# Performance work log

Hardware: AMD Instinct MI355X
Metric: run time of the kernel (lower is better)

The kernel has to match this reference:

```python
import jax, jax.numpy as jnp
import numpy as np

N, H, K, T, B, IN_DIM, L = 1024, 64, 2, 12, 8, 2, 2
NNZ = 16384  # N * avg_degree(16)
M = 2 * K + 1  # supports_len * max_diffusion_step + 1 = 5


def setup_inputs() -> dict:
    key = jax.random.key(0)
    ks = jax.random.split(key, 13)

    def xavier(k, shape):
        std = 1.414 * (2.0 / (shape[0] + shape[1])) ** 0.5
        return std * jax.random.normal(k, shape, dtype=jnp.float32)

    F0 = IN_DIM + H  # 66
    F1 = 2 * H       # 128
    return {
        "inputs": jax.random.normal(ks[0], (T, B, N * IN_DIM), dtype=jnp.float32),
        "initial_hidden_state": jnp.zeros((L, B, N * H), dtype=jnp.float32),
        "support_rows": jax.random.randint(ks[1], (2, NNZ), 0, N, dtype=jnp.int32),
        "support_cols": jax.random.randint(ks[2], (2, NNZ), 0, N, dtype=jnp.int32),
        # scale like a random-walk-normalized adjacency (avg degree ~16)
        "support_vals": jax.random.uniform(ks[3], (2, NNZ), dtype=jnp.float32) / 16.0,
        "Wg0": xavier(ks[4], (F0 * M, 2 * H)),
        "bg0": 0.01 * jax.random.normal(ks[5], (2 * H,), dtype=jnp.float32),
        "Wc0": xavier(ks[6], (F0 * M, H)),
        "bc0": 0.01 * jax.random.normal(ks[7], (H,), dtype=jnp.float32),
        "Wg1": xavier(ks[8], (F1 * M, 2 * H)),
        "bg1": 0.01 * jax.random.normal(ks[9], (2 * H,), dtype=jnp.float32),
        "Wc1": xavier(ks[10], (F1 * M, H)),
        "bc1": 0.01 * jax.random.normal(ks[11], (H,), dtype=jnp.float32),
    }


def reference(inputs, initial_hidden_state, support_rows, support_cols, support_vals,
              Wg0, bg0, Wc0, bc0, Wg1, bg1, Wc1, bc1):
    supports = [(support_rows[i], support_cols[i], support_vals[i])
                for i in range(support_rows.shape[0])]

    def spmm(rows, cols, vals, x):  # sparse [N,N] @ x[N,FB]
        return jax.ops.segment_sum(vals[:, None] * x[cols], rows, num_segments=N)

    def diffuse(x):  # x: [B, N, F] -> [B*N, F*M] (Chebyshev-style recurrence)
        Bz, _, F = x.shape
        x0 = x.transpose(1, 2, 0).reshape(N, F * Bz)
        mats = [x0]
        for rows, cols, vals in supports:
            x1 = spmm(rows, cols, vals, x0)
            mats.append(x1)
            xkm2, xkm1 = x0, x1
            for _ in range(2, K + 1):
                xk = 2.0 * spmm(rows, cols, vals, xkm1) - xkm2
                mats.append(xk)
                xkm2, xkm1 = xkm1, xk
        Xs = jnp.stack(mats, 0).reshape(len(mats), N, F, Bz)
        return Xs.transpose(3, 1, 2, 0).reshape(Bz * N, F * len(mats))

    def cell(params, inp_t, state):  # one DCGRU step
        Wg, bg, Wc, bc = params
        Bz = inp_t.shape[0]
        xi = inp_t.reshape(Bz, N, -1)
        gates = jax.nn.sigmoid(
            diffuse(jnp.concatenate([xi, state.reshape(Bz, N, H)], 2)) @ Wg + bg
        ).reshape(Bz, N, 2 * H)
        r = gates[..., :H].reshape(Bz, N * H)
        u = gates[..., H:].reshape(Bz, N * H)
        cand_in = jnp.concatenate([xi, (r * state).reshape(Bz, N, H)], 2)
        c = jnp.tanh((diffuse(cand_in) @ Wc + bc).reshape(Bz, N * H))
        return u * state + (1.0 - u) * c

    layer_params = [(Wg0, bg0, Wc0, bc0), (Wg1, bg1, Wc1, bc1)]
    cur = inputs  # [T, B, N*input_dim]
    hiddens = []
    for l, params in enumerate(layer_params):
        def step(state, x_t, params=params):
            ns = cell(params, x_t, state)
            return ns, ns
        h_last, outs = jax.lax.scan(step, initial_hidden_state[l], cur)
        hiddens.append(h_last)
        cur = outs  # [T, B, N*H]
    return jnp.stack(hiddens, 0), cur
```

## Files before the change

kernel.cpp:

```cpp
#include <hip/hip_runtime.h>
#include <hip/hip_bf16.h>
#include <math.h>

#define NN 1024
#define HH 64
#define TT 12
#define BB 8
#define INDIM 2
#define LL 2
#define NNZE 16384
#define MM 5

#define FP0 96
#define FP1 128
#define CP0 (BB * FP0)
#define CP1 (BB * FP1)

static constexpr size_t BNH = (size_t)BB * NN * HH;

typedef short bf16x8 __attribute__((ext_vector_type(8)));
typedef float f32x4 __attribute__((ext_vector_type(4)));

__device__ __forceinline__ void fma4(float4& acc, float v, const float4& p) {
  acc.x += v * p.x;
  acc.y += v * p.y;
  acc.z += v * p.z;
  acc.w += v * p.w;
}
__device__ __forceinline__ void mul4(float4& a, const float4& g) {
  a.x *= g.x; a.y *= g.y; a.z *= g.z; a.w *= g.w;
}

__global__ void zero_int_kernel(int* p, int n) {
  int i = blockIdx.x * blockDim.x + threadIdx.x;
  if (i < n) p[i] = 0;
}

__global__ void copy_kernel(const float* __restrict__ src, float* __restrict__ dst, int n) {
  int i = blockIdx.x * blockDim.x + threadIdx.x;
  if (i < n) dst[i] = src[i];
}

__global__ void csr_count_kernel(const int* __restrict__ rows, int* __restrict__ counts) {
  int i = blockIdx.x * blockDim.x + threadIdx.x;
  if (i < 2 * NNZE) {
    int s = i / NNZE;
    atomicAdd(&counts[s * NN + rows[i]], 1);
  }
}

__global__ void csr_scan_kernel(const int* __restrict__ counts, int* __restrict__ row_start,
                                int* __restrict__ cursor) {
  __shared__ int bufA[NN];
  __shared__ int bufB[NN];
  int s = blockIdx.x;
  int t = threadIdx.x;
  bufA[t] = counts[s * NN + t];
  __syncthreads();
  int* src = bufA;
  int* dst = bufB;
  for (int off = 1; off < NN; off <<= 1) {
    dst[t] = src[t] + (t >= off ? src[t - off] : 0);
    __syncthreads();
    int* tmp = src; src = dst; dst = tmp;
  }
  row_start[s * (NN + 1) + t + 1] = src[t];
  cursor[s * NN + t] = (t == 0) ? 0 : src[t - 1];
  if (t == 0) row_start[s * (NN + 1)] = 0;
}

__global__ void csr_scatter_kernel(const int* __restrict__ rows, const int* __restrict__ colsIn,
                                   const float* __restrict__ valsIn, int* __restrict__ cursor,
                                   int* __restrict__ colsOut, float* __restrict__ valsOut) {
  int i = blockIdx.x * blockDim.x + threadIdx.x;
  if (i < 2 * NNZE) {
    int s = i / NNZE;
    int r = rows[i];
    int pos = atomicAdd(&cursor[s * NN + r], 1);
    colsOut[s * NNZE + pos] = colsIn[i];
    valsOut[s * NNZE + pos] = valsIn[i];
  }
}

__global__ void permwT_kernel(const float* __restrict__ W, unsigned short* __restrict__ WTh,
                              unsigned short* __restrict__ WTl, int F, int Fp, int J, int reord) {
  int Ktot = MM * Fp;
  int total = J * Ktot;
  for (int idx = blockIdx.x * blockDim.x + threadIdx.x; idx < total;
       idx += gridDim.x * blockDim.x) {
    int k = idx % Ktot;
    int j = idx / Ktot;
    int m = k / Fp;
    int fn = k - m * Fp;
    int fo;
    if (reord) {
      fo = (fn < HH) ? fn + INDIM : (fn < HH + INDIM ? fn - HH : -1);
    } else {
      fo = (fn < F) ? fn : -1;
    }
    float x = (fo >= 0) ? W[(size_t)(fo * MM + m) * J + j] : 0.f;
    unsigned u = __float_as_uint(x);
    WTh[idx] = (unsigned short)(u >> 16);
    float hf = __uint_as_float(u & 0xFFFF0000u);
    WTl[idx] = (unsigned short)(__float_as_uint(x - hf) >> 16);
  }
}

__global__ __launch_bounds__(256) void spmm1_l1_kernel(
    const int* __restrict__ row_start, const int* __restrict__ cols,
    const float* __restrict__ vals, const float* __restrict__ xi,
    const float* __restrict__ state,
    float* __restrict__ mats) {
  const int r = blockIdx.x, s = blockIdx.y, tid = threadIdx.x;
  const int b = tid >> 5;
  const int f = (tid & 31) * 4;
  const bool isX = (f < HH);
  const float* src = isX ? xi : state;
  const float* sb = src + (size_t)b * NN * HH + (isX ? f : f - HH);

  const int* rs = row_start + s * (NN + 1);
  const int* cs = cols + s * NNZE;
  const float* vs = vals + s * NNZE;
  const int start = rs[r], end = rs[r + 1];

  float4 a0 = {0, 0, 0, 0}, a1 = {0, 0, 0, 0}, a2 = {0, 0, 0, 0}, a3 = {0, 0, 0, 0};
  int e = start;
  for (; e + 3 < end; e += 4) {
    int c0 = cs[e], c1 = cs[e + 1], c2 = cs[e + 2], c3 = cs[e + 3];
    float v0 = vs[e], v1 = vs[e + 1], v2 = vs[e + 2], v3 = vs[e + 3];
    float4 x0 = *(const float4*)(sb + (size_t)c0 * HH);
    float4 x1 = *(const float4*)(sb + (size_t)c1 * HH);
    float4 x2 = *(const float4*)(sb + (size_t)c2 * HH);
    float4 x3 = *(const float4*)(sb + (size_t)c3 * HH);
    fma4(a0, v0, x0); fma4(a1, v1, x1); fma4(a2, v2, x2); fma4(a3, v3, x3);
  }
  for (; e < end; ++e) {
    int c0 = cs[e];
    float v0 = vs[e];
    float4 x0 = *(const float4*)(sb + (size_t)c0 * HH);
    fma4(a0, v0, x0);
  }
  float4 o;
  o.x = (a0.x + a1.x) + (a2.x + a3.x);
  o.y = (a0.y + a1.y) + (a2.y + a3.y);
  o.z = (a0.z + a1.z) + (a2.z + a3.z);
  o.w = (a0.w + a1.w) + (a2.w + a3.w);
  *(float4*)(mats + (size_t)(1 + 2 * s) * (NN * CP1) + (size_t)r * CP1 + tid * 4) = o;

  if (s == 0) {
    *(float4*)(mats + (size_t)r * CP1 + tid * 4) = *(const float4*)(sb + (size_t)r * HH);
  }
}

__global__ __launch_bounds__(256) void spmm1_l0_kernel(
    const int* __restrict__ row_start, const int* __restrict__ cols,
    const float* __restrict__ vals, const float* __restrict__ xi,
    const float* __restrict__ state,
    float* __restrict__ mats) {
  const int tid = threadIdx.x;
  constexpr int SLOTS = FP0 / 4;
  if (tid >= BB * SLOTS) return;
  const int r = blockIdx.x, s = blockIdx.y;
  const int b = tid / SLOTS;
  const int fn = (tid - b * SLOTS) * 4;
  const int c4 = b * FP0 + fn;

  float* x1p = mats + (size_t)(1 + 2 * s) * (NN * CP0) + (size_t)r * CP0 + c4;
  float* x0p = mats + (size_t)r * CP0 + c4;

  const int* rs = row_start + s * (NN + 1);
  const int* cs = cols + s * NNZE;
  const float* vs = vals + s * NNZE;
  const int start = rs[r], end = rs[r + 1];

  if (fn < HH) {
    const float* sb = state + (size_t)b * NN * HH + fn;
    float4 a0 = {0, 0, 0, 0}, a1 = {0, 0, 0, 0}, a2 = {0, 0, 0, 0}, a3 = {0, 0, 0, 0};
    int e = start;
    for (; e + 3 < end; e += 4) {
      int c0 = cs[e], c1 = cs[e + 1], c2 = cs[e + 2], c3 = cs[e + 3];
      float v0 = vs[e], v1 = vs[e + 1], v2 = vs[e + 2], v3 = vs[e + 3];
      float4 x0 = *(const float4*)(sb + (size_t)c0 * HH);
      float4 x1 = *(const float4*)(sb + (size_t)c1 * HH);
      float4 x2 = *(const float4*)(sb + (size_t)c2 * HH);
      float4 x3 = *(const float4*)(sb + (size_t)c3 * HH);
      fma4(a0, v0, x0); fma4(a1, v1, x1); fma4(a2, v2, x2); fma4(a3, v3, x3);
    }
    for (; e < end; ++e) {
      int c0 = cs[e];
      float v0 = vs[e];
      float4 x0 = *(const float4*)(sb + (size_t)c0 * HH);
      fma4(a0, v0, x0);
    }
    float4 o;
    o.x = (a0.x + a1.x) + (a2.x + a3.x);
    o.y = (a0.y + a1.y) + (a2.y + a3.y);
    o.z = (a0.z + a1.z) + (a2.z + a3.z);
    o.w = (a0.w + a1.w) + (a2.w + a3.w);
    *(float4*)x1p = o;
    if (s == 0) *(float4*)x0p = *(const float4*)(sb + (size_t)r * HH);
  } else if (fn == HH) {
    const float* xb = xi + (size_t)b * NN * INDIM;
    float p0 = 0.f, p1 = 0.f, q0 = 0.f, q1 = 0.f;
    int e = start;
    for (; e + 1 < end; e += 2) {
      int c0 = cs[e], c1 = cs[e + 1];
      float v0 = vs[e], v1 = vs[e + 1];
      p0 += v0 * xb[(size_t)c0 * INDIM];
      q0 += v0 * xb[(size_t)c0 * INDIM + 1];
      p1 += v1 * xb[(size_t)c1 * INDIM];
      q1 += v1 * xb[(size_t)c1 * INDIM + 1];
    }
    if (e < end) {
      int c0 = cs[e];
      float v0 = vs[e];
      p0 += v0 * xb[(size_t)c0 * INDIM];
      q0 += v0 * xb[(size_t)c0 * INDIM + 1];
    }
    float4 o = {p0 + p1, q0 + q1, 0.f, 0.f};
    *(float4*)x1p = o;
    if (s == 0) {
      float4 x = {xb[(size_t)r * INDIM], xb[(size_t)r * INDIM + 1], 0.f, 0.f};
      *(float4*)x0p = x;
    }
  } else {
    float4 z = {0, 0, 0, 0};
    *(float4*)x1p = z;
    if (s == 0) *(float4*)x0p = z;
  }
}

template <int LAYER>
__global__ __launch_bounds__(256) void spmm1_state_kernel(
    const int* __restrict__ row_start, const int* __restrict__ cols,
    const float* __restrict__ vals, const float* __restrict__ state,
    const float* __restrict__ gates, float* __restrict__ mats) {
  constexpr int FPP = (LAYER == 0) ? FP0 : FP1;
  constexpr int CP = BB * FPP;
  constexpr int BASE = (LAYER == 0) ? 0 : HH;
  const int tid = threadIdx.x;
  const int r = blockIdx.x * 2 + (tid >> 7);
  const int slot = tid & 127;
  const int b = slot >> 4;
  const int fi = (slot & 15) * 4;
  const int s = blockIdx.y;

  const float* sb = state + (size_t)b * NN * HH + fi;
  const float* gb = gates + (size_t)b * NN * (2 * HH) + fi;

  const int* rs = row_start + s * (NN + 1);
  const int* cs = cols + s * NNZE;
  const float* vs = vals + s * NNZE;
  const int start = rs[r], end = rs[r + 1];

  float4 a0 = {0, 0, 0, 0}, a1 = {0, 0, 0, 0}, a2 = {0, 0, 0, 0}, a3 = {0, 0, 0, 0};
  int e = start;
  for (; e + 3 < end; e += 4) {
    int c0 = cs[e], c1 = cs[e + 1], c2 = cs[e + 2], c3 = cs[e + 3];
    float v0 = vs[e], v1 = vs[e + 1], v2 = vs[e + 2], v3 = vs[e + 3];
    float4 x0 = *(const float4*)(sb + (size_t)c0 * HH);
    float4 g0 = *(const float4*)(gb + (size_t)c0 * (2 * HH));
    float4 x1 = *(const float4*)(sb + (size_t)c1 * HH);
    float4 g1 = *(const float4*)(gb + (size_t)c1 * (2 * HH));
    float4 x2 = *(const float4*)(sb + (size_t)c2 * HH);
    float4 g2 = *(const float4*)(gb + (size_t)c2 * (2 * HH));
    float4 x3 = *(const float4*)(sb + (size_t)c3 * HH);
    float4 g3 = *(const float4*)(gb + (size_t)c3 * (2 * HH));
    mul4(x0, g0); mul4(x1, g1); mul4(x2, g2); mul4(x3, g3);
    fma4(a0, v0, x0); fma4(a1, v1, x1); fma4(a2, v2, x2); fma4(a3, v3, x3);
  }
  for (; e < end; ++e) {
    int c0 = cs[e];
    float v0 = vs[e];
    float4 x0 = *(const float4*)(sb + (size_t)c0 * HH);
    float4 g0 = *(const float4*)(gb + (size_t)c0 * (2 * HH));
    mul4(x0, g0);
    fma4(a0, v0, x0);
  }
  float4 o;
  o.x = (a0.x + a1.x) + (a2.x + a3.x);
  o.y = (a0.y + a1.y) + (a2.y + a3.y);
  o.z = (a0.z + a1.z) + (a2.z + a3.z);
  o.w = (a0.w + a1.w) + (a2.w + a3.w);
  const int c4 = b * FPP + BASE + fi;
  *(float4*)(mats + (size_t)(1 + 2 * s) * (NN * CP) + (size_t)r * CP + c4) = o;

  if (s == 0) {
    float4 x = *(const float4*)(sb + (size_t)r * HH);
    float4 g = *(const float4*)(gb + (size_t)r * (2 * HH));
    mul4(x, g);
    *(float4*)(mats + (size_t)r * CP + c4) = x;
  }
}

template <int LAYER>
__global__ __launch_bounds__(256) void spmm2_kernel(
    const int* __restrict__ row_start, const int* __restrict__ cols,
    const float* __restrict__ vals, float* __restrict__ mats) {
  constexpr int FPP = (LAYER == 0) ? FP0 : FP1;
  constexpr int CPX = BB * FPP;
  const int tid = threadIdx.x;
  int c4, fn;
  if (LAYER == 0) {
    constexpr int SLOTS = FP0 / 4;
    if (tid >= BB * SLOTS) return;
    const int b = tid / SLOTS;
    fn = (tid - b * SLOTS) * 4;
    c4 = b * FP0 + fn;
  } else {
    c4 = tid * 4;
    fn = c4 & (FP1 - 1);
  }
  const int r = blockIdx.x, s = blockIdx.y;
  const size_t NC = (size_t)NN * CPX;
  float* xout = mats + (size_t)(2 + 2 * s) * NC + (size_t)r * CPX + c4;

  if (LAYER == 0 && fn >= HH + 4) {
    float4 z = {0, 0, 0, 0};
    *(float4*)xout = z;
    return;
  }

  const float* xin = mats + (size_t)(1 + 2 * s) * NC + c4;
  const int* rs = row_start + s * (NN + 1);
  const int* cs = cols + s * NNZE;
  const float* vs = vals + s * NNZE;
  const int start = rs[r], end = rs[r + 1];

  float4 a0 = {0, 0, 0, 0}, a1 = {0, 0, 0, 0}, a2 = {0, 0, 0, 0}, a3 = {0, 0, 0, 0};
  int e = start;
  for (; e + 3 < end; e += 4) {
    int c0 = cs[e], c1 = cs[e + 1], c2 = cs[e + 2], c3 = cs[e + 3];
    float v0 = vs[e], v1 = vs[e + 1], v2 = vs[e + 2], v3 = vs[e + 3];
    float4 x0 = *(const float4*)(xin + (size_t)c0 * CPX);
    float4 x1 = *(const float4*)(xin + (size_t)c1 * CPX);
    float4 x2 = *(const float4*)(xin + (size_t)c2 * CPX);
    float4 x3 = *(const float4*)(xin + (size_t)c3 * CPX);
    fma4(a0, v0, x0); fma4(a1, v1, x1); fma4(a2, v2, x2); fma4(a3, v3, x3);
  }
  for (; e < end; ++e) {
    int c0 = cs[e];
    float v0 = vs[e];
    float4 x0 = *(const float4*)(xin + (size_t)c0 * CPX);
    fma4(a0, v0, x0);
  }
  float4 p = *(const float4*)(mats + (size_t)r * CPX + c4);
  float4 o;
  o.x = 2.f * ((a0.x + a1.x) + (a2.x + a3.x)) - p.x;
  o.y = 2.f * ((a0.y + a1.y) + (a2.y + a3.y)) - p.y;
  o.z = 2.f * ((a0.z + a1.z) + (a2.z + a3.z)) - p.z;
  o.w = 2.f * ((a0.w + a1.w) + (a2.w + a3.w)) - p.w;
  *(float4*)xout = o;
}

template <int LAYER>
__global__ __launch_bounds__(256) void spmm2_state_kernel(
    const int* __restrict__ row_start, const int* __restrict__ cols,
    const float* __restrict__ vals, float* __restrict__ mats) {
  constexpr int FPP = (LAYER == 0) ? FP0 : FP1;
  constexpr int CP = BB * FPP;
  constexpr int BASE = (LAYER == 0) ? 0 : HH;
  const int tid = threadIdx.x;
  const int r = blockIdx.x * 2 + (tid >> 7);
  const int slot = tid & 127;
  const int b = slot >> 4;
  const int fi = (slot & 15) * 4;
  const int s = blockIdx.y;
  const int c4 = b * FPP + BASE + fi;
  const size_t NC = (size_t)NN * CP;

  const float* xin = mats + (size_t)(1 + 2 * s) * NC + c4;
  const int* rs = row_start + s * (NN + 1);
  const int* cs = cols + s * NNZE;
  const float* vs = vals + s * NNZE;
  const int start = rs[r], end = rs[r + 1];

  float4 a0 = {0, 0, 0, 0}, a1 = {0, 0, 0, 0}, a2 = {0, 0, 0, 0}, a3 = {0, 0, 0, 0};
  int e = start;
  for (; e + 3 < end; e += 4) {
    int c0 = cs[e], c1 = cs[e + 1], c2 = cs[e + 2], c3 = cs[e + 3];
    float v0 = vs[e], v1 = vs[e + 1], v2 = vs[e + 2], v3 = vs[e + 3];
    float4 x0 = *(const float4*)(xin + (size_t)c0 * CP);
    float4 x1 = *(const float4*)(xin + (size_t)c1 * CP);
    float4 x2 = *(const float4*)(xin + (size_t)c2 * CP);
    float4 x3 = *(const float4*)(xin + (size_t)c3 * CP);
    fma4(a0, v0, x0); fma4(a1, v1, x1); fma4(a2, v2, x2); fma4(a3, v3, x3);
  }
  for (; e < end; ++e) {
    int c0 = cs[e];
    float v0 = vs[e];
    float4 x0 = *(const float4*)(xin + (size_t)c0 * CP);
    fma4(a0, v0, x0);
  }
  float4 p = *(const float4*)(mats + (size_t)r * CP + c4);
  float4 o;
  o.x = 2.f * ((a0.x + a1.x) + (a2.x + a3.x)) - p.x;
  o.y = 2.f * ((a0.y + a1.y) + (a2.y + a3.y)) - p.y;
  o.z = 2.f * ((a0.z + a1.z) + (a2.z + a3.z)) - p.z;
  o.w = 2.f * ((a0.w + a1.w) + (a2.w + a3.w)) - p.w;
  *(float4*)(mats + (size_t)(2 + 2 * s) * NC + (size_t)r * CP + c4) = o;
}

template <int MODE, int BM, int FPP, int JJ>
__global__ __launch_bounds__(256) void gemm_mfma_kernel(
    const float* __restrict__ mats, const unsigned short* __restrict__ WTh,
    const unsigned short* __restrict__ WTl, const float* __restrict__ bias,
    float* __restrict__ gatesOut, const float* __restrict__ gatesIn,
    float* __restrict__ state, float* __restrict__ outT) {
  constexpr int KT = 32;
  constexpr int LDR = 56;
  constexpr int CP = BB * FPP;
  constexpr int KTOT = MM * FPP;
  constexpr int NPH = KTOT / KT;
  constexpr int WTC = (BM == 64) ? 2 : 1;

  __shared__ unsigned short As[2][2][BM][LDR];
  __shared__ unsigned short Ws[2][2][64][LDR];

  const int tid = threadIdx.x;
  const int lane = tid & 63;
  const int wid = tid >> 6;
  const int wr = (BM == 64) ? (wid >> 1) * 32 : 0;
  const int wc = (BM == 64) ? (wid & 1) * 32 : wid * 16;
  const int lr = lane & 15, g = lane >> 4;

  const int bn0 = blockIdx.x * BM;
  const int jb0 = blockIdx.y * 64;
  const int nB = bn0 >> 10;
  const int n0 = bn0 & (NN - 1);

  const int srow = tid >> 2;
  const int scol = (tid & 3) * 8;
  const bool doA = (BM == 64) || (tid < 128);

  float av[8];
  uint4 wh, wl;

  auto gload = [&](int ph) {
    const int m = (ph * KT) / FPP;
    const int f0 = (ph * KT) - m * FPP;
    if (doA) {
      const float* ab =
          mats + (size_t)m * NN * CP + (size_t)(n0 + srow) * CP + nB * FPP + f0 + scol;
      *(float4*)&av[0] = *(const float4*)ab;
      *(float4*)&av[4] = *(const float4*)(ab + 4);
    }
    const size_t woff = (size_t)(jb0 + srow) * KTOT + ph * KT + scol;
    wh = *(const uint4*)(WTh + woff);
    wl = *(const uint4*)(WTl + woff);
  };
  auto stos = [&](int buf) {
    if (doA) {
      unsigned short h8[8], l8[8];
#pragma unroll
      for (int q = 0; q < 8; ++q) {
        float x = av[q];
        unsigned u = __float_as_uint(x);
        h8[q] = (unsigned short)(u >> 16);
        float hf = __uint_as_float(u & 0xFFFF0000u);
        l8[q] = (unsigned short)(__float_as_uint(x - hf) >> 16);
      }
      *(uint4*)&As[buf][0][srow][scol] = *(uint4*)h8;
      *(uint4*)&As[buf][1][srow][scol] = *(uint4*)l8;
    }
    *(uint4*)&Ws[buf][0][srow][scol] = wh;
    *(uint4*)&Ws[buf][1][srow][scol] = wl;
  };

  f32x4 acc[2][WTC] = {};

  auto domfma = [&](int cur) {
    bf16x8 a[2][2], b[WTC][2];
#pragma unroll
    for (int tr = 0; tr < 2; ++tr)
#pragma unroll
      for (int pl = 0; pl < 2; ++pl)
        a[tr][pl] = *(const bf16x8*)&As[cur][pl][wr + tr * 16 + lr][g * 8];
#pragma unroll
    for (int tc = 0; tc < WTC; ++tc)
#pragma unroll
      for (int pl = 0; pl < 2; ++pl)
        b[tc][pl] = *(const bf16x8*)&Ws[cur][pl][wc + tc * 16 + lr][g * 8];
#pragma unroll
    for (int tr = 0; tr < 2; ++tr)
#pragma unroll
      for (int tc = 0; tc < WTC; ++tc) {
        acc[tr][tc] =
            __builtin_amdgcn_mfma_f32_16x16x32_bf16(a[tr][0], b[tc][0], acc[tr][tc], 0, 0, 0);
        acc[tr][tc] =
            __builtin_amdgcn_mfma_f32_16x16x32_bf16(a[tr][0], b[tc][1], acc[tr][tc], 0, 0, 0);
        acc[tr][tc] =
            __builtin_amdgcn_mfma_f32_16x16x32_bf16(a[tr][1], b[tc][0], acc[tr][tc], 0, 0, 0);
      }
  };

  gload(0);
  stos(0);
  __syncthreads();

  for (int ph = 0; ph < NPH; ++ph) {
    const int cur = ph & 1;
    if (ph + 1 < NPH) gload(ph + 1);
    domfma(cur);
    if (ph + 1 < NPH) {
      stos(cur ^ 1);
      __syncthreads();
    }
  }

#pragma unroll
  for (int tr = 0; tr < 2; ++tr)
#pragma unroll
    for (int tc = 0; tc < WTC; ++tc) {
      const int jj = jb0 + wc + tc * 16 + lr;
      const float bs = bias[jj];
#pragma unroll
      for (int q = 0; q < 4; ++q) {
        const int bn = bn0 + wr + tr * 16 + g * 4 + q;
        float v = acc[tr][tc][q] + bs;
        if (MODE == 0) {
          gatesOut[(size_t)bn * (2 * HH) + jj] = 1.f / (1.f + expf(-v));
        } else {
          const int n = bn & (NN - 1);
          const int b = bn >> 10;
          float c = tanhf(v);
          float u = gatesIn[(size_t)bn * (2 * HH) + HH + jj];
          size_t si = (size_t)b * (NN * HH) + (size_t)n * HH + jj;
          float s = state[si];
          float ns = u * s + (1.f - u) * c;
          state[si] = ns;
          outT[si] = ns;
        }
      }
    }
}

extern "C" void kernel_launch(void* const* d_in, const int* in_sizes, int n_in, void* d_out,
                              int out_size, void* d_ws, size_t ws_size, hipStream_t stream) {
  const float* inputs = (const float*)d_in[0];
  const float* init_h = (const float*)d_in[1];
  const int* sup_rows = (const int*)d_in[2];
  const int* sup_cols = (const int*)d_in[3];
  const float* sup_vals = (const float*)d_in[4];
  const float* Wg[2] = {(const float*)d_in[5], (const float*)d_in[9]};
  const float* bg[2] = {(const float*)d_in[6], (const float*)d_in[10]};
  const float* Wc[2] = {(const float*)d_in[7], (const float*)d_in[11]};
  const float* bc[2] = {(const float*)d_in[8], (const float*)d_in[12]};

  float* out_h = (float*)d_out;
  float* out_cur = out_h + (size_t)LL * BNH;

  char* p = (char*)d_ws;
  auto alloc = [&](size_t bytes) -> void* {
    void* r = (void*)p;
    p += (bytes + 255) & ~(size_t)255;
    return r;
  };
  int* colsS = (int*)alloc(2 * NNZE * sizeof(int));
  float* valsS = (float*)alloc(2 * NNZE * sizeof(float));
  int* row_start = (int*)alloc(2 * (NN + 1) * sizeof(int));
  int* cursor = (int*)alloc(2 * NN * sizeof(int));
  int* counts = (int*)alloc(2 * NN * sizeof(int));
  const int K0 = MM * FP0, K1 = MM * FP1;
  unsigned short* WgTh[2];
  unsigned short* WgTl[2];
  unsigned short* WcTh[2];
  unsigned short* WcTl[2];
  WgTh[0] = (unsigned short*)alloc((size_t)128 * K0 * 2);
  WgTl[0] = (unsigned short*)alloc((size_t)128 * K0 * 2);
  WcTh[0] = (unsigned short*)alloc((size_t)64 * K0 * 2);
  WcTl[0] = (unsigned short*)alloc((size_t)64 * K0 * 2);
  WgTh[1] = (unsigned short*)alloc((size_t)128 * K1 * 2);
  WgTl[1] = (unsigned short*)alloc((size_t)128 * K1 * 2);
  WcTh[1] = (unsigned short*)alloc((size_t)64 * K1 * 2);
  WcTl[1] = (unsigned short*)alloc((size_t)64 * K1 * 2);
  float* mats = (float*)alloc((size_t)MM * NN * CP1 * sizeof(float));
  float* gatesBuf = (float*)alloc((size_t)BB * NN * 128 * sizeof(float));
  float* x01 = (float*)alloc(BNH * sizeof(float));

  zero_int_kernel<<<(2 * NN + 255) / 256, 256, 0, stream>>>(counts, 2 * NN);
  csr_count_kernel<<<(2 * NNZE + 255) / 256, 256, 0, stream>>>(sup_rows, counts);
  csr_scan_kernel<<<2, NN, 0, stream>>>(counts, row_start, cursor);
  csr_scatter_kernel<<<(2 * NNZE + 255) / 256, 256, 0, stream>>>(sup_rows, sup_cols, sup_vals,
                                                                 cursor, colsS, valsS);
  permwT_kernel<<<(128 * K0 + 255) / 256, 256, 0, stream>>>(Wg[0], WgTh[0], WgTl[0], 66, FP0, 128, 1);
  permwT_kernel<<<(64 * K0 + 255) / 256, 256, 0, stream>>>(Wc[0], WcTh[0], WcTl[0], 66, FP0, 64, 1);
  permwT_kernel<<<(128 * K1 + 255) / 256, 256, 0, stream>>>(Wg[1], WgTh[1], WgTl[1], 128, FP1, 128, 0);
  permwT_kernel<<<(64 * K1 + 255) / 256, 256, 0, stream>>>(Wc[1], WcTh[1], WcTl[1], 128, FP1, 64, 0);
  copy_kernel<<<((int)(LL * BNH) + 255) / 256, 256, 0, stream>>>(init_h, out_h, (int)(LL * BNH));

  for (int t = 0; t < TT; ++t) {
    {
      float* state = out_h;
      const float* xi = inputs + (size_t)t * BB * NN * INDIM;
      float* outT = x01;
      spmm1_l0_kernel<<<dim3(NN, 2), 256, 0, stream>>>(row_start, colsS, valsS, xi, state, mats);
      spmm2_kernel<0><<<dim3(NN, 2), 256, 0, stream>>>(row_start, colsS, valsS, mats);
      gemm_mfma_kernel<0, 32, FP0, 128><<<dim3(BB * NN / 32, 2), 256, 0, stream>>>(
          mats, WgTh[0], WgTl[0], bg[0], gatesBuf, nullptr, nullptr, nullptr);
      spmm1_state_kernel<0><<<dim3(NN / 2, 2), 256, 0, stream>>>(row_start, colsS, valsS, state,
                                                                 gatesBuf, mats);
      spmm2_state_kernel<0><<<dim3(NN / 2, 2), 256, 0, stream>>>(row_start, colsS, valsS, mats);
      gemm_mfma_kernel<1, 32, FP0, 64><<<dim3(BB * NN / 32, 1), 256, 0, stream>>>(
          mats, WcTh[0], WcTl[0], bc[0], nullptr, gatesBuf, state, outT);
    }
    {
      float* state = out_h + BNH;
      const float* xi = x01;
      float* outT = out_cur + (size_t)t * BNH;
      spmm1_l1_kernel<<<dim3(NN, 2), 256, 0, stream>>>(row_start, colsS, valsS, xi, state, mats);
      spmm2_kernel<1><<<dim3(NN, 2), 256, 0, stream>>>(row_start, colsS, valsS, mats);
      gemm_mfma_kernel<0, 32, FP1, 128><<<dim3(BB * NN / 32, 2), 256, 0, stream>>>(
          mats, WgTh[1], WgTl[1], bg[1], gatesBuf, nullptr, nullptr, nullptr);
      spmm1_state_kernel<1><<<dim3(NN / 2, 2), 256, 0, stream>>>(row_start, colsS, valsS, state,
                                                                 gatesBuf, mats);
      spmm2_state_kernel<1><<<dim3(NN / 2, 2), 256, 0, stream>>>(row_start, colsS, valsS, mats);
      gemm_mfma_kernel<1, 32, FP1, 64><<<dim3(BB * NN / 32, 1), 256, 0, stream>>>(
          mats, WcTh[1], WcTl[1], bc[1], nullptr, gatesBuf, state, outT);
    }
  }
}
```

Measured before the change: 1.877 ms.

## Store diffusion matrices and states in bf16 and fuse r*state into gate GEMM

```diff
diff --git a/kernel.cpp b/kernel.cpp
--- a/kernel.cpp
+++ b/kernel.cpp
@@ -21,24 +21,37 @@
 typedef short bf16x8 __attribute__((ext_vector_type(8)));
 typedef float f32x4 __attribute__((ext_vector_type(4)));
 
-__device__ __forceinline__ void fma4(float4& acc, float v, const float4& p) {
-  acc.x += v * p.x;
-  acc.y += v * p.y;
-  acc.z += v * p.z;
-  acc.w += v * p.w;
-}
-__device__ __forceinline__ void mul4(float4& a, const float4& g) {
-  a.x *= g.x; a.y *= g.y; a.z *= g.z; a.w *= g.w;
+__device__ __forceinline__ unsigned short f2bf(float x) {
+  unsigned u = __float_as_uint(x);
+  u += 0x7FFFu + ((u >> 16) & 1u);
+  return (unsigned short)(u >> 16);
+}
+__device__ __forceinline__ float bf2f(unsigned short h) {
+  return __uint_as_float(((unsigned)h) << 16);
+}
+__device__ __forceinline__ void fma8_bf(float* acc, float v, uint4 pk) {
+  const unsigned short* h = (const unsigned short*)&pk;
+#pragma unroll
+  for (int q = 0; q < 8; ++q) acc[q] += v * bf2f(h[q]);
+}
+__device__ __forceinline__ uint4 pack8(const float* a) {
+  unsigned short h[8];
+#pragma unroll
+  for (int q = 0; q < 8; ++q) h[q] = f2bf(a[q]);
+  return *(const uint4*)h;
 }
 
 __global__ void zero_int_kernel(int* p, int n) {
   int i = blockIdx.x * blockDim.x + threadIdx.x;
   if (i < n) p[i] = 0;
 }
-
 __global__ void copy_kernel(const float* __restrict__ src, float* __restrict__ dst, int n) {
   int i = blockIdx.x * blockDim.x + threadIdx.x;
   if (i < n) dst[i] = src[i];
+}
+__global__ void cvt_kernel(const float* __restrict__ src, unsigned short* __restrict__ dst, int n) {
+  int i = blockIdx.x * blockDim.x + threadIdx.x;
+  if (i < n) dst[i] = f2bf(src[i]);
 }
 
 __global__ void csr_count_kernel(const int* __restrict__ rows, int* __restrict__ counts) {
@@ -48,7 +61,6 @@
     atomicAdd(&counts[s * NN + rows[i]], 1);
   }
 }
-
 __global__ void csr_scan_kernel(const int* __restrict__ counts, int* __restrict__ row_start,
                                 int* __restrict__ cursor) {
   __shared__ int bufA[NN];
@@ -68,7 +80,6 @@
   cursor[s * NN + t] = (t == 0) ? 0 : src[t - 1];
   if (t == 0) row_start[s * (NN + 1)] = 0;
 }
-
 __global__ void csr_scatter_kernel(const int* __restrict__ rows, const int* __restrict__ colsIn,
                                    const float* __restrict__ valsIn, int* __restrict__ cursor,
                                    int* __restrict__ colsOut, float* __restrict__ valsOut) {
@@ -108,320 +119,283 @@
 
 __global__ __launch_bounds__(256) void spmm1_l1_kernel(
     const int* __restrict__ row_start, const int* __restrict__ cols,
-    const float* __restrict__ vals, const float* __restrict__ xi,
-    const float* __restrict__ state,
-    float* __restrict__ mats) {
-  const int r = blockIdx.x, s = blockIdx.y, tid = threadIdx.x;
-  const int b = tid >> 5;
-  const int f = (tid & 31) * 4;
-  const bool isX = (f < HH);
-  const float* src = isX ? xi : state;
-  const float* sb = src + (size_t)b * NN * HH + (isX ? f : f - HH);
+    const float* __restrict__ vals, const unsigned short* __restrict__ xiB,
+    const unsigned short* __restrict__ stateB, unsigned short* __restrict__ matsB) {
+  const int tid = threadIdx.x;
+  const int r = blockIdx.x * 2 + (tid >> 7);
+  const int slot = tid & 127;
+  const int s = blockIdx.y;
+  const int b = slot >> 4;
+  const int f8 = (slot & 15) * 8;
+  const bool isX = (f8 < HH);
+  const unsigned short* sb = (isX ? xiB : stateB) + (size_t)b * NN * HH + (isX ? f8 : f8 - HH);
 
   const int* rs = row_start + s * (NN + 1);
   const int* cs = cols + s * NNZE;
   const float* vs = vals + s * NNZE;
   const int start = rs[r], end = rs[r + 1];
 
-  float4 a0 = {0, 0, 0, 0}, a1 = {0, 0, 0, 0}, a2 = {0, 0, 0, 0}, a3 = {0, 0, 0, 0};
+  float a0[8] = {}, a1[8] = {}, a2[8] = {}, a3[8] = {};
   int e = start;
   for (; e + 3 < end; e += 4) {
     int c0 = cs[e], c1 = cs[e + 1], c2 = cs[e + 2], c3 = cs[e + 3];
     float v0 = vs[e], v1 = vs[e + 1], v2 = vs[e + 2], v3 = vs[e + 3];
-    float4 x0 = *(const float4*)(sb + (size_t)c0 * HH);
-    float4 x1 = *(const float4*)(sb + (size_t)c1 * HH);
-    float4 x2 = *(const float4*)(sb + (size_t)c2 * HH);
-    float4 x3 = *(const float4*)(sb + (size_t)c3 * HH);
-    fma4(a0, v0, x0); fma4(a1, v1, x1); fma4(a2, v2, x2); fma4(a3, v3, x3);
+    uint4 p0 = *(const uint4*)(sb + (size_t)c0 * HH);
+    uint4 p1 = *(const uint4*)(sb + (size_t)c1 * HH);
+    uint4 p2 = *(const uint4*)(sb + (size_t)c2 * HH);
+    uint4 p3 = *(const uint4*)(sb + (size_t)c3 * HH);
+    fma8_bf(a0, v0, p0); fma8_bf(a1, v1, p1); fma8_bf(a2, v2, p2); fma8_bf(a3, v3, p3);
   }
   for (; e < end; ++e) {
-    int c0 = cs[e];
-    float v0 = vs[e];
-    float4 x0 = *(const float4*)(sb + (size_t)c0 * HH);
-    fma4(a0, v0, x0);
-  }
-  float4 o;
-  o.x = (a0.x + a1.x) + (a2.x + a3.x);
-  o.y = (a0.y + a1.y) + (a2.y + a3.y);
-  o.z = (a0.z + a1.z) + (a2.z + a3.z);
-  o.w = (a0.w + a1.w) + (a2.w + a3.w);
-  *(float4*)(mats + (size_t)(1 + 2 * s) * (NN * CP1) + (size_t)r * CP1 + tid * 4) = o;
+    uint4 p0 = *(const uint4*)(sb + (size_t)cs[e] * HH);
+    fma8_bf(a0, vs[e], p0);
+  }
+  float o[8];
+#pragma unroll
+  for (int q = 0; q < 8; ++q) o[q] = (a0[q] + a1[q]) + (a2[q] + a3[q]);
+  *(uint4*)(matsB + (size_t)(1 + 2 * s) * (NN * CP1) + (size_t)r * CP1 + slot * 8) = pack8(o);
 
   if (s == 0) {
-    *(float4*)(mats + (size_t)r * CP1 + tid * 4) = *(const float4*)(sb + (size_t)r * HH);
+    *(uint4*)(matsB + (size_t)r * CP1 + slot * 8) = *(const uint4*)(sb + (size_t)r * HH);
   }
 }
 
 __global__ __launch_bounds__(256) void spmm1_l0_kernel(
     const int* __restrict__ row_start, const int* __restrict__ cols,
-    const float* __restrict__ vals, const float* __restrict__ xi,
-    const float* __restrict__ state,
-    float* __restrict__ mats) {
+    const float* __restrict__ vals, const unsigned short* __restrict__ xiB,
+    const unsigned short* __restrict__ stateB,
+    unsigned short* __restrict__ matsB) {
   const int tid = threadIdx.x;
-  constexpr int SLOTS = FP0 / 4;
-  if (tid >= BB * SLOTS) return;
-  const int r = blockIdx.x, s = blockIdx.y;
-  const int b = tid / SLOTS;
-  const int fn = (tid - b * SLOTS) * 4;
-  const int c4 = b * FP0 + fn;
-
-  float* x1p = mats + (size_t)(1 + 2 * s) * (NN * CP0) + (size_t)r * CP0 + c4;
-  float* x0p = mats + (size_t)r * CP0 + c4;
+  const int slot = tid & 127;
+  constexpr int SLOTS_PB = FP0 / 8;
+  if (slot >= 96) return;
+  const int r = blockIdx.x * 2 + (tid >> 7);
+  const int s = blockIdx.y;
+  const int b = slot / SLOTS_PB;
+  const int f8 = (slot - b * SLOTS_PB) * 8;
+  const int c8 = b * FP0 + f8;
+
+  unsigned short* x1p = matsB + (size_t)(1 + 2 * s) * (NN * CP0) + (size_t)r * CP0 + c8;
+  unsigned short* x0p = matsB + (size_t)r * CP0 + c8;
 
   const int* rs = row_start + s * (NN + 1);
   const int* cs = cols + s * NNZE;
   const float* vs = vals + s * NNZE;
   const int start = rs[r], end = rs[r + 1];
 
-  if (fn < HH) {
-    const float* sb = state + (size_t)b * NN * HH + fn;
-    float4 a0 = {0, 0, 0, 0}, a1 = {0, 0, 0, 0}, a2 = {0, 0, 0, 0}, a3 = {0, 0, 0, 0};
+  if (f8 < HH) {
+    const unsigned short* sb = stateB + (size_t)b * NN * HH + f8;
+    float a0[8] = {}, a1[8] = {}, a2[8] = {}, a3[8] = {};
     int e = start;
     for (; e + 3 < end; e += 4) {
       int c0 = cs[e], c1 = cs[e + 1], c2 = cs[e + 2], c3 = cs[e + 3];
       float v0 = vs[e], v1 = vs[e + 1], v2 = vs[e + 2], v3 = vs[e + 3];
-      float4 x0 = *(const float4*)(sb + (size_t)c0 * HH);
-      float4 x1 = *(const float4*)(sb + (size_t)c1 * HH);
-      float4 x2 = *(const float4*)(sb + (size_t)c2 * HH);
-      float4 x3 = *(const float4*)(sb + (size_t)c3 * HH);
-      fma4(a0, v0, x0); fma4(a1, v1, x1); fma4(a2, v2, x2); fma4(a3, v3, x3);
+      uint4 p0 = *(const uint4*)(sb + (size_t)c0 * HH);
+      uint4 p1 = *(const uint4*)(sb + (size_t)c1 * HH);
+      uint4 p2 = *(const uint4*)(sb + (size_t)c2 * HH);
+      uint4 p3 = *(const uint4*)(sb + (size_t)c3 * HH);
+      fma8_bf(a0, v0, p0); fma8_bf(a1, v1, p1); fma8_bf(a2, v2, p2); fma8_bf(a3, v3, p3);
     }
     for (; e < end; ++e) {
-      int c0 = cs[e];
-      float v0 = vs[e];
-      float4 x0 = *(const float4*)(sb + (size_t)c0 * HH);
-      fma4(a0, v0, x0);
-    }
-    float4 o;
-    o.x = (a0.x + a1.x) + (a2.x + a3.x);
-    o.y = (a0.y + a1.y) + (a2.y + a3.y);
-    o.z = (a0.z + a1.z) + (a2.z + a3.z);
-    o.w = (a0.w + a1.w) + (a2.w + a3.w);
-    *(float4*)x1p = o;
-    if (s == 0) *(float4*)x0p = *(const float4*)(sb + (size_t)r * HH);
-  } else if (fn == HH) {
-    const float* xb = xi + (size_t)b * NN * INDIM;
-    float p0 = 0.f, p1 = 0.f, q0 = 0.f, q1 = 0.f;
+      uint4 p0 = *(const uint4*)(sb + (size_t)cs[e] * HH);
+      fma8_bf(a0, vs[e], p0);
+    }
+    float o[8];
+#pragma unroll
+    for (int q = 0; q < 8; ++q) o[q] = (a0[q] + a1[q]) + (a2[q] + a3[q]);
+    *(uint4*)x1p = pack8(o);
+    if (s == 0) *(uint4*)x0p = *(const uint4*)(sb + (size_t)r * HH);
+  } else if (f8 == HH) {
+    const unsigned short* xb = xiB + (size_t)b * NN * INDIM;
+    float p0 = 0.f, q0 = 0.f, p1 = 0.f, q1 = 0.f;
     int e = start;
     for (; e + 1 < end; e += 2) {
-      int c0 = cs[e], c1 = cs[e + 1];
+      unsigned w0 = *(const unsigned*)(xb + (size_t)cs[e] * INDIM);
+      unsigned w1 = *(const unsigned*)(xb + (size_t)cs[e + 1] * INDIM);
       float v0 = vs[e], v1 = vs[e + 1];
-      p0 += v0 * xb[(size_t)c0 * INDIM];
-      q0 += v0 * xb[(size_t)c0 * INDIM + 1];
-      p1 += v1 * xb[(size_t)c1 * INDIM];
-      q1 += v1 * xb[(size_t)c1 * INDIM + 1];
+      p0 += v0 * bf2f((unsigned short)(w0 & 0xFFFF));
+      q0 += v0 * bf2f((unsigned short)(w0 >> 16));
+      p1 += v1 * bf2f((unsigned short)(w1 & 0xFFFF));
+      q1 += v1 * bf2f((unsigned short)(w1 >> 16));
     }
     if (e < end) {
-      int c0 = cs[e];
+      unsigned w0 = *(const unsigned*)(xb + (size_t)cs[e] * INDIM);
       float v0 = vs[e];
-      p0 += v0 * xb[(size_t)c0 * INDIM];
-      q0 += v0 * xb[(size_t)c0 * INDIM + 1];
-    }
-    float4 o = {p0 + p1, q0 + q1, 0.f, 0.f};
-    *(float4*)x1p = o;
+      p0 += v0 * bf2f((unsigned short)(w0 & 0xFFFF));
+      q0 += v0 * bf2f((unsigned short)(w0 >> 16));
+    }
+    unsigned short h[8] = {f2bf(p0 + p1), f2bf(q0 + q1), 0, 0, 0, 0, 0, 0};
+    *(uint4*)x1p = *(const uint4*)h;
     if (s == 0) {
-      float4 x = {xb[(size_t)r * INDIM], xb[(size_t)r * INDIM + 1], 0.f, 0.f};
-      *(float4*)x0p = x;
+      unsigned w = *(const unsigned*)(xb + (size_t)r * INDIM);
+      unsigned short h0[8] = {(unsigned short)(w & 0xFFFF), (unsigned short)(w >> 16),
+                              0, 0, 0, 0, 0, 0};
+      *(uint4*)x0p = *(const uint4*)h0;
     }
   } else {
-    float4 z = {0, 0, 0, 0};
-    *(float4*)x1p = z;
-    if (s == 0) *(float4*)x0p = z;
+    uint4 z = {0, 0, 0, 0};
+    *(uint4*)x1p = z;
+    if (s == 0) *(uint4*)x0p = z;
   }
 }
 
 template <int LAYER>
 __global__ __launch_bounds__(256) void spmm1_state_kernel(
     const int* __restrict__ row_start, const int* __restrict__ cols,
-    const float* __restrict__ vals, const float* __restrict__ state,
-    const float* __restrict__ gates, float* __restrict__ mats) {
+    const float* __restrict__ vals, const unsigned short* __restrict__ rstateB,
+    unsigned short* __restrict__ matsB) {
   constexpr int FPP = (LAYER == 0) ? FP0 : FP1;
   constexpr int CP = BB * FPP;
   constexpr int BASE = (LAYER == 0) ? 0 : HH;
   const int tid = threadIdx.x;
-  const int r = blockIdx.x * 2 + (tid >> 7);
-  const int slot = tid & 127;
-  const int b = slot >> 4;
-  const int fi = (slot & 15) * 4;
+  const int r = blockIdx.x * 4 + (tid >> 6);
+  const int slot = tid & 63;
+  const int b = slot >> 3;
+  const int f8 = (slot & 7) * 8;
   const int s = blockIdx.y;
-
-  const float* sb = state + (size_t)b * NN * HH + fi;
-  const float* gb = gates + (size_t)b * NN * (2 * HH) + fi;
+  const unsigned short* rb = rstateB + (size_t)b * NN * HH + f8;
 
   const int* rs = row_start + s * (NN + 1);
   const int* cs = cols + s * NNZE;
   const float* vs = vals + s * NNZE;
   const int start = rs[r], end = rs[r + 1];
 
-  float4 a0 = {0, 0, 0, 0}, a1 = {0, 0, 0, 0}, a2 = {0, 0, 0, 0}, a3 = {0, 0, 0, 0};
+  float a0[8] = {}, a1[8] = {}, a2[8] = {}, a3[8] = {};
   int e = start;
   for (; e + 3 < end; e += 4) {
     int c0 = cs[e], c1 = cs[e + 1], c2 = cs[e + 2], c3 = cs[e + 3];
     float v0 = vs[e], v1 = vs[e + 1], v2 = vs[e + 2], v3 = vs[e + 3];
-    float4 x0 = *(const float4*)(sb + (size_t)c0 * HH);
-    float4 g0 = *(const float4*)(gb + (size_t)c0 * (2 * HH));
-    float4 x1 = *(const float4*)(sb + (size_t)c1 * HH);
-    float4 g1 = *(const float4*)(gb + (size_t)c1 * (2 * HH));
-    float4 x2 = *(const float4*)(sb + (size_t)c2 * HH);
-    float4 g2 = *(const float4*)(gb + (size_t)c2 * (2 * HH));
-    float4 x3 = *(const float4*)(sb + (size_t)c3 * HH);
-    float4 g3 = *(const float4*)(gb + (size_t)c3 * (2 * HH));
-    mul4(x0, g0); mul4(x1, g1); mul4(x2, g2); mul4(x3, g3);
-    fma4(a0, v0, x0); fma4(a1, v1, x1); fma4(a2, v2, x2); fma4(a3, v3, x3);
+    uint4 p0 = *(const uint4*)(rb + (size_t)c0 * HH);
+    uint4 p1 = *(const uint4*)(rb + (size_t)c1 * HH);
+    uint4 p2 = *(const uint4*)(rb + (size_t)c2 * HH);
+    uint4 p3 = *(const uint4*)(rb + (size_t)c3 * HH);
+    fma8_bf(a0, v0, p0); fma8_bf(a1, v1, p1); fma8_bf(a2, v2, p2); fma8_bf(a3, v3, p3);
   }
   for (; e < end; ++e) {
-    int c0 = cs[e];
-    float v0 = vs[e];
-    float4 x0 = *(const float4*)(sb + (size_t)c0 * HH);
-    float4 g0 = *(const float4*)(gb + (size_t)c0 * (2 * HH));
-    mul4(x0, g0);
-    fma4(a0, v0, x0);
-  }
-  float4 o;
-  o.x = (a0.x + a1.x) + (a2.x + a3.x);
-  o.y = (a0.y + a1.y) + (a2.y + a3.y);
-  o.z = (a0.z + a1.z) + (a2.z + a3.z);
-  o.w = (a0.w + a1.w) + (a2.w + a3.w);
-  const int c4 = b * FPP + BASE + fi;
-  *(float4*)(mats + (size_t)(1 + 2 * s) * (NN * CP) + (size_t)r * CP + c4) = o;
+    uint4 p0 = *(const uint4*)(rb + (size_t)cs[e] * HH);
+    fma8_bf(a0, vs[e], p0);
+  }
+  float o[8];
+#pragma unroll
+  for (int q = 0; q < 8; ++q) o[q] = (a0[q] + a1[q]) + (a2[q] + a3[q]);
+  const int c8 = b * FPP + BASE + f8;
+  *(uint4*)(matsB + (size_t)(1 + 2 * s) * (NN * CP) + (size_t)r * CP + c8) = pack8(o);
 
   if (s == 0) {
-    float4 x = *(const float4*)(sb + (size_t)r * HH);
-    float4 g = *(const float4*)(gb + (size_t)r * (2 * HH));
-    mul4(x, g);
-    *(float4*)(mats + (size_t)r * CP + c4) = x;
+    *(uint4*)(matsB + (size_t)r * CP + c8) = *(const uint4*)(rb + (size_t)r * HH);
   }
 }
 
 template <int LAYER>
 __global__ __launch_bounds__(256) void spmm2_kernel(
     const int* __restrict__ row_start, const int* __restrict__ cols,
-    const float* __restrict__ vals, float* __restrict__ mats) {
+    const float* __restrict__ vals, unsigned short* __restrict__ matsB) {
   constexpr int FPP = (LAYER == 0) ? FP0 : FP1;
-  constexpr int CPX = BB * FPP;
+  constexpr int CP = BB * FPP;
+  constexpr int SLOTS = CP / 8;
   const int tid = threadIdx.x;
-  int c4, fn;
-  if (LAYER == 0) {
-    constexpr int SLOTS = FP0 / 4;
-    if (tid >= BB * SLOTS) return;
-    const int b = tid / SLOTS;
-    fn = (tid - b * SLOTS) * 4;
-    c4 = b * FP0 + fn;
-  } else {
-    c4 = tid * 4;
-    fn = c4 & (FP1 - 1);
-  }
-  const int r = blockIdx.x, s = blockIdx.y;
-  const size_t NC = (size_t)NN * CPX;
-  float* xout = mats + (size_t)(2 + 2 * s) * NC + (size_t)r * CPX + c4;
-
-  if (LAYER == 0 && fn >= HH + 4) {
-    float4 z = {0, 0, 0, 0};
-    *(float4*)xout = z;
-    return;
-  }
-
-  const float* xin = mats + (size_t)(1 + 2 * s) * NC + c4;
+  const int slot = tid & 127;
+  if (slot >= SLOTS) return;
+  const int r = blockIdx.x * 2 + (tid >> 7);
+  const int s = blockIdx.y;
+  const int c8 = slot * 8;
+  const size_t NC = (size_t)NN * CP;
+  const unsigned short* xin = matsB + (size_t)(1 + 2 * s) * NC + c8;
+
   const int* rs = row_start + s * (NN + 1);
   const int* cs = cols + s * NNZE;
   const float* vs = vals + s * NNZE;
   const int start = rs[r], end = rs[r + 1];
 
-  float4 a0 = {0, 0, 0, 0}, a1 = {0, 0, 0, 0}, a2 = {0, 0, 0, 0}, a3 = {0, 0, 0, 0};
+  float a0[8] = {}, a1[8] = {}, a2[8] = {}, a3[8] = {};
   int e = start;
   for (; e + 3 < end; e += 4) {
     int c0 = cs[e], c1 = cs[e + 1], c2 = cs[e + 2], c3 = cs[e + 3];
     float v0 = vs[e], v1 = vs[e + 1], v2 = vs[e + 2], v3 = vs[e + 3];
-    float4 x0 = *(const float4*)(xin + (size_t)c0 * CPX);
-    float4 x1 = *(const float4*)(xin + (size_t)c1 * CPX);
-    float4 x2 = *(const float4*)(xin + (size_t)c2 * CPX);
-    float4 x3 = *(const float4*)(xin + (size_t)c3 * CPX);
-    fma4(a0, v0, x0); fma4(a1, v1, x1); fma4(a2, v2, x2); fma4(a3, v3, x3);
+    uint4 p0 = *(const uint4*)(xin + (size_t)c0 * CP);
+    uint4 p1 = *(const uint4*)(xin + (size_t)c1 * CP);
+    uint4 p2 = *(const uint4*)(xin + (size_t)c2 * CP);
+    uint4 p3 = *(const uint4*)(xin + (size_t)c3 * CP);
+    fma8_bf(a0, v0, p0); fma8_bf(a1, v1, p1); fma8_bf(a2, v2, p2); fma8_bf(a3, v3, p3);
   }
   for (; e < end; ++e) {
-    int c0 = cs[e];
-    float v0 = vs[e];
-    float4 x0 = *(const float4*)(xin + (size_t)c0 * CPX);
-    fma4(a0, v0, x0);
-  }
-  float4 p = *(const float4*)(mats + (size_t)r * CPX + c4);
-  float4 o;
-  o.x = 2.f * ((a0.x + a1.x) + (a2.x + a3.x)) - p.x;
-  o.y = 2.f * ((a0.y + a1.y) + (a2.y + a3.y)) - p.y;
-  o.z = 2.f * ((a0.z + a1.z) + (a2.z + a3.z)) - p.z;
-  o.w = 2.f * ((a0.w + a1.w) + (a2.w + a3.w)) - p.w;
-  *(float4*)xout = o;
+    uint4 p0 = *(const uint4*)(xin + (size_t)cs[e] * CP);
+    fma8_bf(a0, vs[e], p0);
+  }
+  uint4 x0v = *(const uint4*)(matsB + (size_t)r * CP + c8);
+  const unsigned short* x0h = (const unsigned short*)&x0v;
+  float o[8];
+#pragma unroll
+  for (int q = 0; q < 8; ++q)
+    o[q] = 2.f * ((a0[q] + a1[q]) + (a2[q] + a3[q])) - bf2f(x0h[q]);
+  *(uint4*)(matsB + (size_t)(2 + 2 * s) * NC + (size_t)r * CP + c8) = pack8(o);
 }
 
 template <int LAYER>
 __global__ __launch_bounds__(256) void spmm2_state_kernel(
     const int* __restrict__ row_start, const int* __restrict__ cols,
-    const float* __restrict__ vals, float* __restrict__ mats) {
+    const float* __restrict__ vals, unsigned short* __restrict__ matsB) {
   constexpr int FPP = (LAYER == 0) ? FP0 : FP1;
   constexpr int CP = BB * FPP;
   constexpr int BASE = (LAYER == 0) ? 0 : HH;
   const int tid = threadIdx.x;
-  const int r = blockIdx.x * 2 + (tid >> 7);
-  const int slot = tid & 127;
-  const int b = slot >> 4;
-  const int fi = (slot & 15) * 4;
+  const int r = blockIdx.x * 4 + (tid >> 6);
+  const int slot = tid & 63;
+  const int b = slot >> 3;
+  const int f8 = (slot & 7) * 8;
   const int s = blockIdx.y;
-  const int c4 = b * FPP + BASE + fi;
+  const int c8 = b * FPP + BASE + f8;
   const size_t NC = (size_t)NN * CP;
-
-  const float* xin = mats + (size_t)(1 + 2 * s) * NC + c4;
+  const unsigned short* xin = matsB + (size_t)(1 + 2 * s) * NC + c8;
+
   const int* rs = row_start + s * (NN + 1);
   const int* cs = cols + s * NNZE;
   const float* vs = vals + s * NNZE;
   const int start = rs[r], end = rs[r + 1];
 
-  float4 a0 = {0, 0, 0, 0}, a1 = {0, 0, 0, 0}, a2 = {0, 0, 0, 0}, a3 = {0, 0, 0, 0};
+  float a0[8] = {}, a1[8] = {}, a2[8] = {}, a3[8] = {};
   int e = start;
   for (; e + 3 < end; e += 4) {
     int c0 = cs[e], c1 = cs[e + 1], c2 = cs[e + 2], c3 = cs[e + 3];
     float v0 = vs[e], v1 = vs[e + 1], v2 = vs[e + 2], v3 = vs[e + 3];
-    float4 x0 = *(const float4*)(xin + (size_t)c0 * CP);
-    float4 x1 = *(const float4*)(xin + (size_t)c1 * CP);
-    float4 x2 = *(const float4*)(xin + (size_t)c2 * CP);
-    float4 x3 = *(const float4*)(xin + (size_t)c3 * CP);
-    fma4(a0, v0, x0); fma4(a1, v1, x1); fma4(a2, v2, x2); fma4(a3, v3, x3);
+    uint4 p0 = *(const uint4*)(xin + (size_t)c0 * CP);
+    uint4 p1 = *(const uint4*)(xin + (size_t)c1 * CP);
+    uint4 p2 = *(const uint4*)(xin + (size_t)c2 * CP);
+    uint4 p3 = *(const uint4*)(xin + (size_t)c3 * CP);
+    fma8_bf(a0, v0, p0); fma8_bf(a1, v1, p1); fma8_bf(a2, v2, p2); fma8_bf(a3, v3, p3);
   }
   for (; e < end; ++e) {
-    int c0 = cs[e];
-    float v0 = vs[e];
-    float4 x0 = *(const float4*)(xin + (size_t)c0 * CP);
-    fma4(a0, v0, x0);
-  }
-  float4 p = *(const float4*)(mats + (size_t)r * CP + c4);
-  float4 o;
-  o.x = 2.f * ((a0.x + a1.x) + (a2.x + a3.x)) - p.x;
-  o.y = 2.f * ((a0.y + a1.y) + (a2.y + a3.y)) - p.y;
-  o.z = 2.f * ((a0.z + a1.z) + (a2.z + a3.z)) - p.z;
-  o.w = 2.f * ((a0.w + a1.w) + (a2.w + a3.w)) - p.w;
-  *(float4*)(mats + (size_t)(2 + 2 * s) * NC + (size_t)r * CP + c4) = o;
-}
-
-template <int MODE, int BM, int FPP, int JJ>
+    uint4 p0 = *(const uint4*)(xin + (size_t)cs[e] * CP);
+    fma8_bf(a0, vs[e], p0);
+  }
+  uint4 x0v = *(const uint4*)(matsB + (size_t)r * CP + c8);
+  const unsigned short* x0h = (const unsigned short*)&x0v;
+  float o[8];
+#pragma unroll
+  for (int q = 0; q < 8; ++q)
+    o[q] = 2.f * ((a0[q] + a1[q]) + (a2[q] + a3[q])) - bf2f(x0h[q]);
+  *(uint4*)(matsB + (size_t)(2 + 2 * s) * NC + (size_t)r * CP + c8) = pack8(o);
+}
+
+template <int MODE, int FPP, int JJ>
 __global__ __launch_bounds__(256) void gemm_mfma_kernel(
-    const float* __restrict__ mats, const unsigned short* __restrict__ WTh,
+    const unsigned short* __restrict__ matsB, const unsigned short* __restrict__ WTh,
     const unsigned short* __restrict__ WTl, const float* __restrict__ bias,
-    float* __restrict__ gatesOut, const float* __restrict__ gatesIn,
-    float* __restrict__ state, float* __restrict__ outT) {
-  constexpr int KT = 32;
-  constexpr int LDR = 56;
+    unsigned short* __restrict__ rstateB, float* __restrict__ uBuf, float* __restrict__ state,
+    unsigned short* __restrict__ stateBf, unsigned short* __restrict__ outBf,
+    float* __restrict__ outT) {
+  constexpr int BM = 32, KT = 32, LDR = 40;
   constexpr int CP = BB * FPP;
   constexpr int KTOT = MM * FPP;
   constexpr int NPH = KTOT / KT;
-  constexpr int WTC = (BM == 64) ? 2 : 1;
-
-  __shared__ unsigned short As[2][2][BM][LDR];
+
+  __shared__ unsigned short As[2][BM][LDR];
   __shared__ unsigned short Ws[2][2][64][LDR];
 
   const int tid = threadIdx.x;
   const int lane = tid & 63;
   const int wid = tid >> 6;
-  const int wr = (BM == 64) ? (wid >> 1) * 32 : 0;
-  const int wc = (BM == 64) ? (wid & 1) * 32 : wid * 16;
+  const int wc = wid * 16;
   const int lr = lane & 15, g = lane >> 4;
 
   const int bn0 = blockIdx.x * BM;
@@ -429,69 +403,40 @@
   const int nB = bn0 >> 10;
   const int n0 = bn0 & (NN - 1);
 
-  const int srow = tid >> 2;
-  const int scol = (tid & 3) * 8;
-  const bool doA = (BM == 64) || (tid < 128);
-
-  float av[8];
-  uint4 wh, wl;
+  const int arow = tid >> 2;
+  const int acol = (tid & 3) * 8;
+  const bool doA = (tid < 128);
+
+  uint4 aval, wh, wl;
 
   auto gload = [&](int ph) {
     const int m = (ph * KT) / FPP;
     const int f0 = (ph * KT) - m * FPP;
     if (doA) {
-      const float* ab =
-          mats + (size_t)m * NN * CP + (size_t)(n0 + srow) * CP + nB * FPP + f0 + scol;
-      *(float4*)&av[0] = *(const float4*)ab;
-      *(float4*)&av[4] = *(const float4*)(ab + 4);
-    }
-    const size_t woff = (size_t)(jb0 + srow) * KTOT + ph * KT + scol;
+      aval = *(const uint4*)(matsB + (size_t)m * NN * CP + (size_t)(n0 + arow) * CP +
+                             nB * FPP + f0 + acol);
+    }
+    const size_t woff = (size_t)(jb0 + arow) * KTOT + ph * KT + acol;
     wh = *(const uint4*)(WTh + woff);
     wl = *(const uint4*)(WTl + woff);
   };
   auto stos = [&](int buf) {
-    if (doA) {
-      unsigned short h8[8], l8[8];
-#pragma unroll
-      for (int q = 0; q < 8; ++q) {
-        float x = av[q];
-        unsigned u = __float_as_uint(x);
-        h8[q] = (unsigned short)(u >> 16);
-        float hf = __uint_as_float(u & 0xFFFF0000u);
-        l8[q] = (unsigned short)(__float_as_uint(x - hf) >> 16);
-      }
-      *(uint4*)&As[buf][0][srow][scol] = *(uint4*)h8;
-      *(uint4*)&As[buf][1][srow][scol] = *(uint4*)l8;
-    }
-    *(uint4*)&Ws[buf][0][srow][scol] = wh;
-    *(uint4*)&Ws[buf][1][srow][scol] = wl;
+    if (doA) *(uint4*)&As[buf][arow][acol] = aval;
+    *(uint4*)&Ws[buf][0][arow][acol] = wh;
+    *(uint4*)&Ws[buf][1][arow][acol] = wl;
   };
 
-  f32x4 acc[2][WTC] = {};
+  f32x4 acc[2] = {};
 
   auto domfma = [&](int cur) {
-    bf16x8 a[2][2], b[WTC][2];
-#pragma unroll
-    for (int tr = 0; tr < 2; ++tr)
-#pragma unroll
-      for (int pl = 0; pl < 2; ++pl)
-        a[tr][pl] = *(const bf16x8*)&As[cur][pl][wr + tr * 16 + lr][g * 8];
-#pragma unroll
-    for (int tc = 0; tc < WTC; ++tc)
-#pragma unroll
-      for (int pl = 0; pl < 2; ++pl)
-        b[tc][pl] = *(const bf16x8*)&Ws[cur][pl][wc + tc * 16 + lr][g * 8];
-#pragma unroll
-    for (int tr = 0; tr < 2; ++tr)
-#pragma unroll
-      for (int tc = 0; tc < WTC; ++tc) {
-        acc[tr][tc] =
-            __builtin_amdgcn_mfma_f32_16x16x32_bf16(a[tr][0], b[tc][0], acc[tr][tc], 0, 0, 0);
-        acc[tr][tc] =
-            __builtin_amdgcn_mfma_f32_16x16x32_bf16(a[tr][0], b[tc][1], acc[tr][tc], 0, 0, 0);
-        acc[tr][tc] =
-            __builtin_amdgcn_mfma_f32_16x16x32_bf16(a[tr][1], b[tc][0], acc[tr][tc], 0, 0, 0);
-      }
+    bf16x8 a0 = *(const bf16x8*)&As[cur][0 * 16 + lr][g * 8];
+    bf16x8 a1 = *(const bf16x8*)&As[cur][1 * 16 + lr][g * 8];
+    bf16x8 bh = *(const bf16x8*)&Ws[cur][0][wc + lr][g * 8];
+    bf16x8 bl = *(const bf16x8*)&Ws[cur][1][wc + lr][g * 8];
+    acc[0] = __builtin_amdgcn_mfma_f32_16x16x32_bf16(a0, bh, acc[0], 0, 0, 0);
+    acc[0] = __builtin_amdgcn_mfma_f32_16x16x32_bf16(a0, bl, acc[0], 0, 0, 0);
+    acc[1] = __builtin_amdgcn_mfma_f32_16x16x32_bf16(a1, bh, acc[1], 0, 0, 0);
+    acc[1] = __builtin_amdgcn_mfma_f32_16x16x32_bf16(a1, bl, acc[1], 0, 0, 0);
   };
 
   gload(0);
@@ -508,31 +453,37 @@
     }
   }
 
-#pragma unroll
-  for (int tr = 0; tr < 2; ++tr)
-#pragma unroll
-    for (int tc = 0; tc < WTC; ++tc) {
-      const int jj = jb0 + wc + tc * 16 + lr;
-      const float bs = bias[jj];
-#pragma unroll
-      for (int q = 0; q < 4; ++q) {
-        const int bn = bn0 + wr + tr * 16 + g * 4 + q;
-        float v = acc[tr][tc][q] + bs;
-        if (MODE == 0) {
-          gatesOut[(size_t)bn * (2 * HH) + jj] = 1.f / (1.f + expf(-v));
+  const int jj = jb0 + wc + lr;
+  const float bs = bias[jj];
+#pragma unroll
+  for (int tr = 0; tr < 2; ++tr) {
+#pragma unroll
+    for (int q = 0; q < 4; ++q) {
+      const int bn = bn0 + tr * 16 + g * 4 + q;
+      const int n = bn & (NN - 1);
+      const int b = bn >> 10;
+      float v = acc[tr][q] + bs;
+      if (MODE == 0) {
+        float sg = 1.f / (1.f + expf(-v));
+        if (jj < HH) {
+          size_t si = (size_t)b * (NN * HH) + (size_t)n * HH + jj;
+          rstateB[si] = f2bf(sg * state[si]);
         } else {
-          const int n = bn & (NN - 1);
-          const int b = bn >> 10;
-          float c = tanhf(v);
-          float u = gatesIn[(size_t)bn * (2 * HH) + HH + jj];
-          size_t si = (size_t)b * (NN * HH) + (size_t)n * HH + jj;
-          float s = state[si];
-          float ns = u * s + (1.f - u) * c;
-          state[si] = ns;
-          outT[si] = ns;
+          uBuf[(size_t)bn * HH + (jj - HH)] = sg;
         }
+      } else {
+        float c = tanhf(v);
+        float u = uBuf[(size_t)bn * HH + jj];
+        size_t si = (size_t)b * (NN * HH) + (size_t)n * HH + jj;
+        float s = state[si];
+        float ns = u * s + (1.f - u) * c;
+        state[si] = ns;
+        stateBf[si] = f2bf(ns);
+        if (outBf) outBf[si] = f2bf(ns);
+        if (outT) outT[si] = ns;
       }
     }
+  }
 }
 
 extern "C" void kernel_launch(void* const* d_in, const int* in_sizes, int n_in, void* d_out,
@@ -562,10 +513,8 @@
   int* cursor = (int*)alloc(2 * NN * sizeof(int));
   int* counts = (int*)alloc(2 * NN * sizeof(int));
   const int K0 = MM * FP0, K1 = MM * FP1;
-  unsigned short* WgTh[2];
-  unsigned short* WgTl[2];
-  unsigned short* WcTh[2];
-  unsigned short* WcTl[2];
+  unsigned short* WgTh[2]; unsigned short* WgTl[2];
+  unsigned short* WcTh[2]; unsigned short* WcTl[2];
   WgTh[0] = (unsigned short*)alloc((size_t)128 * K0 * 2);
   WgTl[0] = (unsigned short*)alloc((size_t)128 * K0 * 2);
   WcTh[0] = (unsigned short*)alloc((size_t)64 * K0 * 2);
@@ -574,9 +523,14 @@
   WgTl[1] = (unsigned short*)alloc((size_t)128 * K1 * 2);
   WcTh[1] = (unsigned short*)alloc((size_t)64 * K1 * 2);
   WcTl[1] = (unsigned short*)alloc((size_t)64 * K1 * 2);
-  float* mats = (float*)alloc((size_t)MM * NN * CP1 * sizeof(float));
-  float* gatesBuf = (float*)alloc((size_t)BB * NN * 128 * sizeof(float));
-  float* x01 = (float*)alloc(BNH * sizeof(float));
+  unsigned short* matsB = (unsigned short*)alloc((size_t)MM * NN * CP1 * 2);
+  unsigned short* stateBf = (unsigned short*)alloc(2 * BNH * 2);
+  unsigned short* x01Bf = (unsigned short*)alloc(BNH * 2);
+  unsigned short* rstateB = (unsigned short*)alloc(BNH * 2);
+  float* uBuf = (float*)alloc(BNH * sizeof(float));
+  unsigned short* inputsBf = (unsigned short*)alloc((size_t)TT * BB * NN * INDIM * 2);
+  unsigned short* stateBf0 = stateBf;
+  unsigned short* stateBf1 = stateBf + BNH;
 
   zero_int_kernel<<<(2 * NN + 255) / 256, 256, 0, stream>>>(counts, 2 * NN);
   csr_count_kernel<<<(2 * NNZE + 255) / 256, 256, 0, stream>>>(sup_rows, counts);
@@ -588,35 +542,38 @@
   permwT_kernel<<<(128 * K1 + 255) / 256, 256, 0, stream>>>(Wg[1], WgTh[1], WgTl[1], 128, FP1, 128, 0);
   permwT_kernel<<<(64 * K1 + 255) / 256, 256, 0, stream>>>(Wc[1], WcTh[1], WcTl[1], 128, FP1, 64, 0);
   copy_kernel<<<((int)(LL * BNH) + 255) / 256, 256, 0, stream>>>(init_h, out_h, (int)(LL * BNH));
+  cvt_kernel<<<((int)(2 * BNH) + 255) / 256, 256, 0, stream>>>(init_h, stateBf, (int)(2 * BNH));
+  cvt_kernel<<<(TT * BB * NN * INDIM + 255) / 256, 256, 0, stream>>>(
+      inputs, inputsBf, TT * BB * NN * INDIM);
 
   for (int t = 0; t < TT; ++t) {
     {
       float* state = out_h;
-      const float* xi = inputs + (size_t)t * BB * NN * INDIM;
-      float* outT = x01;
-      spmm1_l0_kernel<<<dim3(NN, 2), 256, 0, stream>>>(row_start, colsS, valsS, xi, state, mats);
-      spmm2_kernel<0><<<dim3(NN, 2), 256, 0, stream>>>(row_start, colsS, valsS, mats);
-      gemm_mfma_kernel<0, 32, FP0, 128><<<dim3(BB * NN / 32, 2), 256, 0, stream>>>(
-          mats, WgTh[0], WgTl[0], bg[0], gatesBuf, nullptr, nullptr, nullptr);
-      spmm1_state_kernel<0><<<dim3(NN / 2, 2), 256, 0, stream>>>(row_start, colsS, valsS, state,
-                                                                 gatesBuf, mats);
-      spmm2_state_kernel<0><<<dim3(NN / 2, 2), 256, 0, stream>>>(row_start, colsS, valsS, mats);
-      gemm_mfma_kernel<1, 32, FP0, 64><<<dim3(BB * NN / 32, 1), 256, 0, stream>>>(
-          mats, WcTh[0], WcTl[0], bc[0], nullptr, gatesBuf, state, outT);
+      const unsigned short* xiB = inputsBf + (size_t)t * BB * NN * INDIM;
+      spmm1_l0_kernel<<<dim3(NN / 2, 2), 256, 0, stream>>>(row_start, colsS, valsS, xiB,
+                                                           stateBf0, matsB);
+      spmm2_kernel<0><<<dim3(NN / 2, 2), 256, 0, stream>>>(row_start, colsS, valsS, matsB);
+      gemm_mfma_kernel<0, FP0, 128><<<dim3(BB * NN / 32, 2), 256, 0, stream>>>(
+          matsB, WgTh[0], WgTl[0], bg[0], rstateB, uBuf, state, nullptr, nullptr, nullptr);
+      spmm1_state_kernel<0><<<dim3(NN / 4, 2), 256, 0, stream>>>(row_start, colsS, valsS,
+                                                                 rstateB, matsB);
+      spmm2_state_kernel<0><<<dim3(NN / 4, 2), 256, 0, stream>>>(row_start, colsS, valsS, matsB);
+      gemm_mfma_kernel<1, FP0, 64><<<dim3(BB * NN / 32, 1), 256, 0, stream>>>(
+          matsB, WcTh[0], WcTl[0], bc[0], nullptr, uBuf, state, stateBf0, x01Bf, nullptr);
     }
     {
       float* state = out_h + BNH;
-      const float* xi = x01;
       float* outT = out_cur + (size_t)t * BNH;
-      spmm1_l1_kernel<<<dim3(NN, 2), 256, 0, stream>>>(row_start, colsS, valsS, xi, state, mats);
-      spmm2_kernel<1><<<dim3(NN, 2), 256, 0, stream>>>(row_start, colsS, valsS, mats);
-      gemm_mfma_kernel<0, 32, FP1, 128><<<dim3(BB * NN / 32, 2), 256, 0, stream>>>(
-          mats, WgTh[1], WgTl[1], bg[1], gatesBuf, nullptr, nullptr, nullptr);
-      spmm1_state_kernel<1><<<dim3(NN / 2, 2), 256, 0, stream>>>(row_start, colsS, valsS, state,
-                                                                 gatesBuf, mats);
-      spmm2_state_kernel<1><<<dim3(NN / 2, 2), 256, 0, stream>>>(row_start, colsS, valsS, mats);
-      gemm_mfma_kernel<1, 32, FP1, 64><<<dim3(BB * NN / 32, 1), 256, 0, stream>>>(
-          mats, WcTh[1], WcTl[1], bc[1], nullptr, gatesBuf, state, outT);
-    }
-  }
-}
+      spmm1_l1_kernel<<<dim3(NN / 2, 2), 256, 0, stream>>>(row_start, colsS, valsS, x01Bf,
+                                                           stateBf1, matsB);
+      spmm2_kernel<1><<<dim3(NN / 2, 2), 256, 0, stream>>>(row_start, colsS, valsS, matsB);
+      gemm_mfma_kernel<0, FP1, 128><<<dim3(BB * NN / 32, 2), 256, 0, stream>>>(
+          matsB, WgTh[1], WgTl[1], bg[1], rstateB, uBuf, state, nullptr, nullptr, nullptr);
+      spmm1_state_kernel<1><<<dim3(NN / 4, 2), 256, 0, stream>>>(row_start, colsS, valsS,
+                                                                 rstateB, matsB);
+      spmm2_state_kernel<1><<<dim3(NN / 4, 2), 256, 0, stream>>>(row_start, colsS, valsS, matsB);
+      gemm_mfma_kernel<1, FP1, 64><<<dim3(BB * NN / 32, 1), 256, 0, stream>>>(
+          matsB, WcTh[1], WcTl[1], bc[1], nullptr, uBuf, state, stateBf1, nullptr, outT);
+    }
+  }
+}
```

Result: faster. 1.817 ms (-3.2%).
